# Kernel optimization log

Measured on AMD Instinct MI355X. Metric: run time of the kernel, lower is better.

Reference implementation:

```python
import jax, jax.numpy as jnp
import numpy as np

N_DELAYS = 512
N_SAMPLES = 2 ** 15  # 32768


def _interp_linear(x, out_size):
    # F.interpolate(mode='linear', align_corners=False) on [B, C, L]
    L = x.shape[-1]
    scale = L / out_size
    pos = (jnp.arange(out_size, dtype=jnp.float32) + 0.5) * scale - 0.5
    pos = jnp.clip(pos, 0.0, L - 1)
    i0 = jnp.floor(pos).astype(jnp.int32)
    i1 = jnp.minimum(i0 + 1, L - 1)
    w = (pos - i0).astype(x.dtype)
    return x[..., i0] * (1.0 - w) + x[..., i1] * w


def _interp_nearest(x, out_size):
    # F.interpolate(mode='nearest') on [B, C, L]: idx = floor(j * L/out)
    L = x.shape[-1]
    idx = jnp.clip(jnp.floor(jnp.arange(out_size) * (L / out_size)).astype(jnp.int32), 0, L - 1)
    return x[..., idx]


def setup_inputs() -> dict:
    key = jax.random.key(0)
    k1, k2, k3, k4, k5 = jax.random.split(key, 5)
    batch = 8
    impulse = jax.random.normal(k1, (batch, 128), dtype=jnp.float32)
    delay_selection = jax.random.normal(k2, (batch, N_DELAYS, 16), dtype=jnp.float32)
    damping = jax.random.normal(k3, (batch, 1), dtype=jnp.float32)
    filt = jax.random.normal(k4, (batch, 16), dtype=jnp.float32)
    # torch forward draws uniform(-1,1) noise; passed as input for determinism
    noise = jax.random.uniform(k5, (batch, 1, N_SAMPLES), dtype=jnp.float32, minval=-1.0, maxval=1.0)
    # comb-filter buffer: delays[i, ::i+1] = 1
    delays_np = np.zeros((N_DELAYS, N_SAMPLES), dtype=np.float32)
    for i in range(N_DELAYS):
        delays_np[i, ::i + 1] = 1.0
    delays = jnp.asarray(delays_np)
    return {"impulse": impulse, "delay_selection": delay_selection, "damping": damping,
            "filt": filt, "noise": noise, "delays": delays}


def reference(impulse, delay_selection, damping, filt, noise, delays):
    batch = delay_selection.shape[0]
    n_delays, n_samples = delays.shape
    n_frames = filt.shape[-1]

    # filter spectrum envelope: sigmoid -> linear upsample to n_samples//2 -> pad 1
    f = jax.nn.sigmoid(filt).reshape(-1, 1, n_frames)
    f = _interp_linear(f, n_samples // 2)
    filt_spec = jnp.pad(f, ((0, 0), (0, 0), (0, 1)))  # [B,1,n_samples//2+1]

    # impulse: squared envelope upsampled, modulating uniform noise
    imp = impulse.reshape(batch, 1, -1) ** 2
    imp = _interp_linear(imp, n_samples) * noise  # [B,1,n_samples]

    # damping: powers = linspace(1, 1, n_frames) == ones (faithful to source)
    damp = jax.nn.sigmoid(damping.reshape(batch, 1)) * 0.9999
    powers = jnp.linspace(1.0, float(damp.shape[-1]), n_frames)
    damp = damp[:, :, None] ** powers[None, None, :]  # [B,1,n_frames]
    damp = _interp_nearest(damp, n_samples)  # [B,1,n_samples]

    # sparse comb selection: softmax over delays, nearest upsample, weighted sum
    ds = jax.nn.softmax(delay_selection.reshape(batch, n_delays, -1), axis=1)
    ds = _interp_nearest(ds, n_samples)  # [B,n_delays,n_samples]
    d = jnp.einsum('bdn,dn->bn', ds, delays)[:, None, :] * damp  # [B,1,n_samples]

    # FFT convolution
    delay_spec = jnp.fft.rfft(d, axis=-1, norm='ortho')
    impulse_spec = jnp.fft.rfft(imp, axis=-1, norm='ortho')
    spec = delay_spec * impulse_spec * filt_spec
    final = jnp.fft.irfft(spec, n=n_samples, axis=-1, norm='ortho')
    return final
```

## Files before the change

kernel.cpp:

```cpp
#include <hip/hip_runtime.h>
#include <math.h>

#define NSAMP 32768
#define NDEL  512
#define NFR   16
#define BATCH 8
#define TWO_PI 6.283185307179586f

__device__ __forceinline__ float2 cmul(float2 a, float2 b) {
    return make_float2(a.x*b.x - a.y*b.y, a.x*b.y + a.y*b.x);
}
__device__ __forceinline__ float2 cadd(float2 a, float2 b){ return make_float2(a.x+b.x, a.y+b.y); }
__device__ __forceinline__ float2 csub(float2 a, float2 b){ return make_float2(a.x-b.x, a.y-b.y); }
__device__ __forceinline__ float2 crot(float2 z, float sign){ return make_float2(-sign*z.y, sign*z.x); }

__device__ __forceinline__ int phi(int i){ return i + (i >> 3); }

__device__ __forceinline__ void bfly8(const float2 v[8], float sign, float2 X[8]) {
    const float S2 = 0.70710678118654752f;
    float2 t0 = cadd(v[0], v[4]), t1 = csub(v[0], v[4]);
    float2 t2 = cadd(v[2], v[6]), t3 = crot(csub(v[2], v[6]), sign);
    float2 E0 = cadd(t0, t2), E1 = cadd(t1, t3), E2 = csub(t0, t2), E3 = csub(t1, t3);
    float2 u0 = cadd(v[1], v[5]), u1 = csub(v[1], v[5]);
    float2 u2 = cadd(v[3], v[7]), u3 = crot(csub(v[3], v[7]), sign);
    float2 O0 = cadd(u0, u2), O1 = cadd(u1, u3), O2 = csub(u0, u2), O3 = csub(u1, u3);
    float2 c1 = make_float2( S2, sign*S2);
    float2 c3 = make_float2(-S2, sign*S2);
    float2 w1o = cmul(c1, O1);
    float2 w2o = crot(O2, sign);
    float2 w3o = cmul(c3, O3);
    X[0]=cadd(E0,O0);  X[4]=csub(E0,O0);
    X[1]=cadd(E1,w1o); X[5]=csub(E1,w1o);
    X[2]=cadd(E2,w2o); X[6]=csub(E2,w2o);
    X[3]=cadd(E3,w3o); X[7]=csub(E3,w3o);
}

__device__ __forceinline__ void twiddle_q(float2 v[8], float ang1) {
    float sa, ca; __sincosf(ang1, &sa, &ca);
    float2 w1 = make_float2(ca, sa), wq = w1;
#pragma unroll
    for (int q = 1; q < 8; ++q) { v[q] = cmul(v[q], wq); wq = cmul(wq, w1); }
}

__global__ void build_kernel(const float* __restrict__ impulse,
                             const float* __restrict__ dsel,
                             const float* __restrict__ damping,
                             const float* __restrict__ noise,
                             float2* __restrict__ At) {
    const int b   = blockIdx.x >> 6;
    const int f   = (blockIdx.x >> 2) & 15;
    const int sub = blockIdx.x & 3;
    const int tid = threadIdx.x;
    __shared__ float Wrow[NDEL];
    __shared__ float dl[512];
    __shared__ float red[64];

    float v[8], m = -1e30f;
#pragma unroll
    for (int k = 0; k < 8; ++k) {
        v[k] = dsel[(b*NDEL + tid + 64*k)*NFR + f];
        m = fmaxf(m, v[k]);
    }
    red[tid] = m;
    __syncthreads();
    for (int off = 32; off > 0; off >>= 1) {
        if (tid < off) red[tid] = fmaxf(red[tid], red[tid+off]);
        __syncthreads();
    }
    float M = red[0];
    __syncthreads();
    float e[8], s = 0.0f;
#pragma unroll
    for (int k = 0; k < 8; ++k) { e[k] = expf(v[k] - M); s += e[k]; }
    red[tid] = s;
    __syncthreads();
    for (int off = 32; off > 0; off >>= 1) {
        if (tid < off) red[tid] += red[tid+off];
        __syncthreads();
    }
    float S = red[0];
    float damp = 1.0f/(1.0f + expf(-damping[b])) * 0.9999f;
    float scale = damp / S;
#pragma unroll
    for (int k = 0; k < 8; ++k) Wrow[tid + 64*k] = e[k] * scale;
    for (int k = tid; k < 512; k += 64) dl[k] = 0.0f;
    __syncthreads();

    const unsigned start = ((unsigned)f << 11) + ((unsigned)sub << 9);
    const float fstart = (float)start;

    for (unsigned t = 1; t < 64; ++t) {
        float wt = Wrow[t-1];
        unsigned q0 = (unsigned)(__fdividef(fstart, (float)t));
        unsigned n0 = q0 * t;
        while (n0 < start) n0 += t;
        while (n0 >= start + t) n0 -= t;
        for (unsigned i = (n0 - start) + (unsigned)tid * t; i < 512u; i += 64u * t)
            atomicAdd(&dl[i], wt);
    }
    for (unsigned t = 64u + (unsigned)tid; t <= 512u; t += 64u) {
        float wt = Wrow[t-1];
        unsigned q0 = (unsigned)(__fdividef(fstart, (float)t));
        unsigned n0 = q0 * t;
        while (n0 < start) n0 += t;
        while (n0 >= start + t) n0 -= t;
        for (unsigned i = n0 - start; i < 512u; i += t)
            atomicAdd(&dl[i], wt);
    }
    __syncthreads();

    const int n1base = (int)(start >> 6);
    float2* op = At + b*NSAMP + tid*512 + n1base;
#pragma unroll
    for (int q = 0; q < 8; ++q) {
        int n = (int)start + tid + 64*q;
        float pos = (n + 0.5f) * (1.0f/256.0f) - 0.5f;
        pos = fminf(fmaxf(pos, 0.0f), 127.0f);
        int i0 = (int)pos;
        float w = pos - (float)i0;
        int i1 = (i0 + 1 > 127) ? 127 : i0 + 1;
        float x0 = impulse[b*128 + i0]; x0 *= x0;
        float x1 = impulse[b*128 + i1]; x1 *= x1;
        float iv = (x0*(1.0f - w) + x1*w) * noise[b*NSAMP + n];
        op[q] = make_float2(dl[tid + 64*q], iv);
    }
}

__global__ void fft512_kernel(const float2* __restrict__ src,
                              float2* __restrict__ dst,
                              const float* __restrict__ filt,
                              float sign) {
    const int j  = threadIdx.x;
    const int s  = blockIdx.x >> 6;
    const int n2 = blockIdx.x & 63;
    __shared__ float2 buf[2][576];
    __shared__ float fs[NFR];
    if (filt && j < NFR)
        fs[j] = 1.0f/(1.0f + expf(-filt[s*NFR + j]));
    __syncthreads();

    const float2* sp = src + s * NSAMP;
    float2 v[8], X[8];
    if (!filt) {
#pragma unroll
        for (int q = 0; q < 8; ++q) v[q] = sp[n2*512 + j + 64*q];
    } else {
        const float SCALE = 1.0f / (32768.0f * 181.01933598375618f);
        const int prow = (64 - n2) & 63;
#pragma unroll
        for (int q = 0; q < 8; ++q) {
            int n1 = j + 64*q;
            int m  = 64*n1 + n2;
            float2 Zk = sp[n2*512 + n1];
            int pcol = n2 ? (511 - n1) : ((512 - n1) & 511);
            float2 Zr = sp[prow*512 + pcol];
            float2 Zrc = make_float2(Zr.x, -Zr.y);
            float2 D = make_float2(0.5f*(Zk.x + Zrc.x), 0.5f*(Zk.y + Zrc.y));
            float2 df = make_float2(Zk.x - Zrc.x, Zk.y - Zrc.y);
            float2 I = make_float2(0.5f*df.y, -0.5f*df.x);
            int jjb = (m <= NSAMP - m) ? m : NSAMP - m;
            float fv = 0.0f;
            if (jjb < NSAMP/2) {
                float pos = (jjb + 0.5f) * (1.0f/1024.0f) - 0.5f;
                pos = fminf(fmaxf(pos, 0.0f), 15.0f);
                int i0 = (int)pos;
                float w = pos - (float)i0;
                int i1 = (i0 + 1 > 15) ? 15 : i0 + 1;
                fv = fs[i0]*(1.0f - w) + fs[i1]*w;
            }
            float2 spc = cmul(D, I);
            float g = fv * SCALE;
            v[q] = make_float2(spc.x * g, spc.y * g);
        }
    }

    bfly8(v, sign, X);
#pragma unroll
    for (int r = 0; r < 8; ++r) buf[0][phi(8*j + r)] = X[r];
    __syncthreads();
#pragma unroll
    for (int q = 0; q < 8; ++q) v[q] = buf[0][phi(j + 64*q)];
    int jm = j & 7;
    twiddle_q(v, sign * TWO_PI * (float)jm * (1.0f/64.0f));
    bfly8(v, sign, X);
#pragma unroll
    for (int r = 0; r < 8; ++r) buf[1][phi(((j>>3)<<6) + jm + (r<<3))] = X[r];
    __syncthreads();
#pragma unroll
    for (int q = 0; q < 8; ++q) v[q] = buf[1][phi(j + 64*q)];
    twiddle_q(v, sign * TWO_PI * (float)j * (1.0f/512.0f));
    bfly8(v, sign, X);

    float2* dp = dst + s * NSAMP + n2 * 512;
#pragma unroll
    for (int r = 0; r < 8; ++r) {
        int k1 = j + 64*r;
        int pr = (n2 * k1) & (NSAMP - 1);
        float sa, ca; __sincosf(sign * TWO_PI * (float)pr * (1.0f/32768.0f), &sa, &ca);
        dp[k1] = cmul(X[r], make_float2(ca, sa));
    }
}

__global__ void fft64_kernel(const float2* __restrict__ src,
                             float2* __restrict__ dstT,
                             float* __restrict__ out_real,
                             float sign) {
    const int l = threadIdx.x;
    const int c = l & 7, jj = l >> 3;
    const int s = blockIdx.x >> 6;
    const int k1base = (blockIdx.x & 63) << 3;
    __shared__ float2 buf[576];

    const float2* sp = src + s * NSAMP;
    float2 v[8], X[8];
#pragma unroll
    for (int q = 0; q < 8; ++q) v[q] = sp[(jj + 8*q)*512 + k1base + c];

    bfly8(v, sign, X);
#pragma unroll
    for (int r = 0; r < 8; ++r) buf[phi(c*64 + jj*8 + r)] = X[r];
    __syncthreads();
#pragma unroll
    for (int q = 0; q < 8; ++q) v[q] = buf[phi(c*64 + jj + 8*q)];
    twiddle_q(v, sign * TWO_PI * (float)jj * (1.0f/64.0f));
    bfly8(v, sign, X);

    const int k1 = k1base + c;
    if (out_real) {
        float* op = out_real + s * NSAMP + k1;
#pragma unroll
        for (int r = 0; r < 8; ++r) op[512*(jj + 8*r)] = X[r].x;
    } else {
        float2* dp = dstT + s * NSAMP + (k1 & 63)*512 + (k1 >> 6) + 8*jj;
#pragma unroll
        for (int r = 0; r < 8; ++r) dp[64*r] = X[r];
    }
}

extern "C" void kernel_launch(void* const* d_in, const int* in_sizes, int n_in,
                              void* d_out, int out_size, void* d_ws, size_t ws_size,
                              hipStream_t stream) {
    const float* impulse = (const float*)d_in[0];
    const float* dsel    = (const float*)d_in[1];
    const float* damping = (const float*)d_in[2];
    const float* filt    = (const float*)d_in[3];
    const float* noise   = (const float*)d_in[4];
    float* out = (float*)d_out;

    float2* A = (float2*)d_ws;
    float2* B = A + BATCH * NSAMP;

    build_kernel<<<dim3(512), dim3(64), 0, stream>>>(impulse, dsel, damping, noise, A);
    fft512_kernel<<<dim3(512), dim3(64), 0, stream>>>(A, B, nullptr, -1.0f);
    fft64_kernel <<<dim3(512), dim3(64), 0, stream>>>(B, A, nullptr, -1.0f);
    fft512_kernel<<<dim3(512), dim3(64), 0, stream>>>(A, B, filt, 1.0f);
    fft64_kernel <<<dim3(512), dim3(64), 0, stream>>>(B, nullptr, out, 1.0f);
}
```

Before: 135.9 us.

## Fuse five FFT-pipeline kernels into one cooperative kernel with grid syncs

Replaces the five separate kernel launches (build, two forward FFT passes, two inverse FFT passes) with a single cooperative kernel that runs each phase as a device function and separates phases with grid-wide syncs. Shared memory is unified into one buffer reused across phases. This removes per-launch overhead and inter-kernel gaps, at the cost of grid barriers and the requirement that all 512 blocks be co-resident.

```diff
diff --git a/kernel.cpp b/kernel.cpp
--- a/kernel.cpp
+++ b/kernel.cpp
@@ -1,5 +1,8 @@
 #include <hip/hip_runtime.h>
+#include <hip/hip_cooperative_groups.h>
 #include <math.h>
+
+namespace cg = cooperative_groups;
 
 #define NSAMP 32768
 #define NDEL  512
@@ -42,18 +45,18 @@
     for (int q = 1; q < 8; ++q) { v[q] = cmul(v[q], wq); wq = cmul(wq, w1); }
 }
 
-__global__ void build_kernel(const float* __restrict__ impulse,
-                             const float* __restrict__ dsel,
-                             const float* __restrict__ damping,
-                             const float* __restrict__ noise,
-                             float2* __restrict__ At) {
-    const int b   = blockIdx.x >> 6;
-    const int f   = (blockIdx.x >> 2) & 15;
-    const int sub = blockIdx.x & 3;
+__device__ void phase_build(int task, const float* __restrict__ impulse,
+                            const float* __restrict__ dsel,
+                            const float* __restrict__ damping,
+                            const float* __restrict__ noise,
+                            float2* __restrict__ At, float2* sbuf) {
+    const int b   = task >> 6;
+    const int f   = (task >> 2) & 15;
+    const int sub = task & 3;
     const int tid = threadIdx.x;
-    __shared__ float Wrow[NDEL];
-    __shared__ float dl[512];
-    __shared__ float red[64];
+    float* Wrow = (float*)sbuf;
+    float* dl   = Wrow + 512;
+    float* red  = dl + 512;
 
     float v[8], m = -1e30f;
 #pragma unroll
@@ -126,15 +129,15 @@
     }
 }
 
-__global__ void fft512_kernel(const float2* __restrict__ src,
-                              float2* __restrict__ dst,
-                              const float* __restrict__ filt,
-                              float sign) {
+__device__ void phase_fft512(int task, const float2* __restrict__ src,
+                             float2* __restrict__ dst,
+                             const float* __restrict__ filt,
+                             float sign, float2* sbuf, float* fs) {
     const int j  = threadIdx.x;
-    const int s  = blockIdx.x >> 6;
-    const int n2 = blockIdx.x & 63;
-    __shared__ float2 buf[2][576];
-    __shared__ float fs[NFR];
+    const int s  = task >> 6;
+    const int n2 = task & 63;
+    float2* buf0 = sbuf;
+    float2* buf1 = sbuf + 576;
     if (filt && j < NFR)
         fs[j] = 1.0f/(1.0f + expf(-filt[s*NFR + j]));
     __syncthreads();
@@ -176,18 +179,18 @@
 
     bfly8(v, sign, X);
 #pragma unroll
-    for (int r = 0; r < 8; ++r) buf[0][phi(8*j + r)] = X[r];
-    __syncthreads();
-#pragma unroll
-    for (int q = 0; q < 8; ++q) v[q] = buf[0][phi(j + 64*q)];
+    for (int r = 0; r < 8; ++r) buf0[phi(8*j + r)] = X[r];
+    __syncthreads();
+#pragma unroll
+    for (int q = 0; q < 8; ++q) v[q] = buf0[phi(j + 64*q)];
     int jm = j & 7;
     twiddle_q(v, sign * TWO_PI * (float)jm * (1.0f/64.0f));
     bfly8(v, sign, X);
 #pragma unroll
-    for (int r = 0; r < 8; ++r) buf[1][phi(((j>>3)<<6) + jm + (r<<3))] = X[r];
-    __syncthreads();
-#pragma unroll
-    for (int q = 0; q < 8; ++q) v[q] = buf[1][phi(j + 64*q)];
+    for (int r = 0; r < 8; ++r) buf1[phi(((j>>3)<<6) + jm + (r<<3))] = X[r];
+    __syncthreads();
+#pragma unroll
+    for (int q = 0; q < 8; ++q) v[q] = buf1[phi(j + 64*q)];
     twiddle_q(v, sign * TWO_PI * (float)j * (1.0f/512.0f));
     bfly8(v, sign, X);
 
@@ -201,15 +204,15 @@
     }
 }
 
-__global__ void fft64_kernel(const float2* __restrict__ src,
-                             float2* __restrict__ dstT,
-                             float* __restrict__ out_real,
-                             float sign) {
+__device__ void phase_fft64(int task, const float2* __restrict__ src,
+                            float2* __restrict__ dstT,
+                            float* __restrict__ out_real,
+                            float sign, float2* sbuf) {
     const int l = threadIdx.x;
     const int c = l & 7, jj = l >> 3;
-    const int s = blockIdx.x >> 6;
-    const int k1base = (blockIdx.x & 63) << 3;
-    __shared__ float2 buf[576];
+    const int s = task >> 6;
+    const int k1base = (task & 63) << 3;
+    float2* buf = sbuf;
 
     const float2* sp = src + s * NSAMP;
     float2 v[8], X[8];
@@ -235,6 +238,27 @@
 #pragma unroll
         for (int r = 0; r < 8; ++r) dp[64*r] = X[r];
     }
+}
+
+__global__ void __launch_bounds__(64)
+fused_kernel(const float* __restrict__ impulse, const float* __restrict__ dsel,
+             const float* __restrict__ damping, const float* __restrict__ filt,
+             const float* __restrict__ noise, float2* __restrict__ A,
+             float2* __restrict__ B, float* __restrict__ out) {
+    cg::grid_group grid = cg::this_grid();
+    __shared__ float2 sbuf[1152];
+    __shared__ float  sfs[NFR];
+    const int task = blockIdx.x;
+
+    phase_build(task, impulse, dsel, damping, noise, A, sbuf);
+    __threadfence(); grid.sync();
+    phase_fft512(task, A, B, nullptr, -1.0f, sbuf, sfs);
+    __threadfence(); grid.sync();
+    phase_fft64(task, B, A, nullptr, -1.0f, sbuf);
+    __threadfence(); grid.sync();
+    phase_fft512(task, A, B, filt, 1.0f, sbuf, sfs);
+    __threadfence(); grid.sync();
+    phase_fft64(task, B, nullptr, out, 1.0f, sbuf);
 }
 
 extern "C" void kernel_launch(void* const* d_in, const int* in_sizes, int n_in,
@@ -250,9 +274,8 @@
     float2* A = (float2*)d_ws;
     float2* B = A + BATCH * NSAMP;
 
-    build_kernel<<<dim3(512), dim3(64), 0, stream>>>(impulse, dsel, damping, noise, A);
-    fft512_kernel<<<dim3(512), dim3(64), 0, stream>>>(A, B, nullptr, -1.0f);
-    fft64_kernel <<<dim3(512), dim3(64), 0, stream>>>(B, A, nullptr, -1.0f);
-    fft512_kernel<<<dim3(512), dim3(64), 0, stream>>>(A, B, filt, 1.0f);
-    fft64_kernel <<<dim3(512), dim3(64), 0, stream>>>(B, nullptr, out, 1.0f);
-}
+    void* args[] = {(void*)&impulse, (void*)&dsel, (void*)&damping, (void*)&filt,
+                    (void*)&noise,   (void*)&A,    (void*)&B,       (void*)&out};
+    hipLaunchCooperativeKernel((const void*)fused_kernel, dim3(512), dim3(64),
+                               args, 0, stream);
+}
```

New measurement: 440.1 us. 224% more time.

## Fuse forward fft64, spectral multiply and inverse fft64 into one kernel

Applied to the files above, without the earlier changes.

Combines the forward 64-point column FFT, the real-signal split and spectrum multiply with the filter envelope, and the inverse 64-point column FFT into a single kernel. Each block pairs columns k with their mirror columns so the conjugate-symmetric partner is available in shared memory. This removes one kernel launch and a full round-trip of the intermediate complex buffer through global memory. The final inverse 512-point FFT now writes the real output directly. The trade-off is more complex indexing and special-case handling for the DC and Nyquist columns, which carries some correctness risk.

```diff
diff --git a/kernel.cpp b/kernel.cpp
--- a/kernel.cpp
+++ b/kernel.cpp
@@ -126,39 +126,101 @@
     }
 }
 
-__global__ void fft512_kernel(const float2* __restrict__ src,
-                              float2* __restrict__ dst,
-                              const float* __restrict__ filt,
-                              float sign) {
+__global__ void fft512_fwd_kernel(const float2* __restrict__ src,
+                                  float2* __restrict__ dst) {
     const int j  = threadIdx.x;
     const int s  = blockIdx.x >> 6;
     const int n2 = blockIdx.x & 63;
     __shared__ float2 buf[2][576];
-    __shared__ float fs[NFR];
-    if (filt && j < NFR)
-        fs[j] = 1.0f/(1.0f + expf(-filt[s*NFR + j]));
-    __syncthreads();
+    const float sign = -1.0f;
 
     const float2* sp = src + s * NSAMP;
     float2 v[8], X[8];
-    if (!filt) {
-#pragma unroll
-        for (int q = 0; q < 8; ++q) v[q] = sp[n2*512 + j + 64*q];
-    } else {
-        const float SCALE = 1.0f / (32768.0f * 181.01933598375618f);
-        const int prow = (64 - n2) & 63;
-#pragma unroll
-        for (int q = 0; q < 8; ++q) {
-            int n1 = j + 64*q;
-            int m  = 64*n1 + n2;
-            float2 Zk = sp[n2*512 + n1];
-            int pcol = n2 ? (511 - n1) : ((512 - n1) & 511);
-            float2 Zr = sp[prow*512 + pcol];
+#pragma unroll
+    for (int q = 0; q < 8; ++q) v[q] = sp[n2*512 + j + 64*q];
+
+    bfly8(v, sign, X);
+#pragma unroll
+    for (int r = 0; r < 8; ++r) buf[0][phi(8*j + r)] = X[r];
+    __syncthreads();
+#pragma unroll
+    for (int q = 0; q < 8; ++q) v[q] = buf[0][phi(j + 64*q)];
+    int jm = j & 7;
+    twiddle_q(v, sign * TWO_PI * (float)jm * (1.0f/64.0f));
+    bfly8(v, sign, X);
+#pragma unroll
+    for (int r = 0; r < 8; ++r) buf[1][phi(((j>>3)<<6) + jm + (r<<3))] = X[r];
+    __syncthreads();
+#pragma unroll
+    for (int q = 0; q < 8; ++q) v[q] = buf[1][phi(j + 64*q)];
+    twiddle_q(v, sign * TWO_PI * (float)j * (1.0f/512.0f));
+    bfly8(v, sign, X);
+
+    float2* dp = dst + s * NSAMP + n2 * 512;
+#pragma unroll
+    for (int r = 0; r < 8; ++r) {
+        int k1 = j + 64*r;
+        int pr = (n2 * k1) & (NSAMP - 1);
+        float sa, ca; __sincosf(sign * TWO_PI * (float)pr * (1.0f/32768.0f), &sa, &ca);
+        dp[k1] = cmul(X[r], make_float2(ca, sa));
+    }
+}
+
+__global__ void mega_kernel(const float2* __restrict__ G,
+                            float2* __restrict__ H,
+                            const float* __restrict__ filt) {
+    const int l  = threadIdx.x;
+    const int cc = l & 7, jj = l >> 3;
+    const int s  = blockIdx.x >> 6;
+    const int g  = blockIdx.x & 63;
+    __shared__ float2 Z[8][65];
+    __shared__ float2 buf[576];
+    __shared__ float fs[NFR];
+    __shared__ int cols[8];
+
+    if (l < NFR) fs[l] = 1.0f/(1.0f + expf(-filt[s*NFR + l]));
+    if (l < 8) {
+        int col;
+        if (l < 4)        col = 4*g + l;
+        else if (g == 0)  col = (l == 4) ? 256 : 512 - (l - 4);
+        else              col = 512 - 4*g - (l - 4);
+        cols[l] = col;
+    }
+    __syncthreads();
+
+    const float2* sp = G + s * NSAMP;
+    const int mycol = cols[cc];
+    float2 v[8], X[8];
+
+#pragma unroll
+    for (int q = 0; q < 8; ++q) v[q] = sp[(jj + 8*q)*512 + mycol];
+    bfly8(v, -1.0f, X);
+#pragma unroll
+    for (int r = 0; r < 8; ++r) buf[phi(cc*64 + jj*8 + r)] = X[r];
+    __syncthreads();
+#pragma unroll
+    for (int q = 0; q < 8; ++q) v[q] = buf[phi(cc*64 + jj + 8*q)];
+    twiddle_q(v, -TWO_PI * (float)jj * (1.0f/64.0f));
+    bfly8(v, -1.0f, X);
+#pragma unroll
+    for (int r = 0; r < 8; ++r) Z[cc][jj + 8*r] = X[r];
+    __syncthreads();
+
+    const float SCALE = 1.0f / (32768.0f * 181.01933598375618f);
+#pragma unroll
+    for (int it = 0; it < 4; ++it) {
+        int c  = l & 3;
+        int k2 = (l >> 2) + 16*it;
+        if (!(g == 0 && c == 0)) {
+            int col = cols[c];
+            float2 Zk = Z[c][k2];
+            float2 Zr = Z[c+4][63 - k2];
             float2 Zrc = make_float2(Zr.x, -Zr.y);
             float2 D = make_float2(0.5f*(Zk.x + Zrc.x), 0.5f*(Zk.y + Zrc.y));
             float2 df = make_float2(Zk.x - Zrc.x, Zk.y - Zrc.y);
             float2 I = make_float2(0.5f*df.y, -0.5f*df.x);
-            int jjb = (m <= NSAMP - m) ? m : NSAMP - m;
+            int k = col + 512*k2;
+            int jjb = (k <= NSAMP - k) ? k : NSAMP - k;
             float fv = 0.0f;
             if (jjb < NSAMP/2) {
                 float pos = (jjb + 0.5f) * (1.0f/1024.0f) - 0.5f;
@@ -168,11 +230,97 @@
                 int i1 = (i0 + 1 > 15) ? 15 : i0 + 1;
                 fv = fs[i0]*(1.0f - w) + fs[i1]*w;
             }
-            float2 spc = cmul(D, I);
-            float g = fv * SCALE;
-            v[q] = make_float2(spc.x * g, spc.y * g);
+            float2 spec = cmul(D, I);
+            float gs = fv * SCALE;
+            Z[c][k2]        = make_float2( spec.x*gs,  spec.y*gs);
+            Z[c+4][63 - k2] = make_float2( spec.x*gs, -spec.y*gs);
         }
     }
+    if (g == 0) {
+        if (l <= 32) {
+            int k2 = l, k2p = (64 - k2) & 63;
+            float2 Zk = Z[0][k2];
+            float2 Zr = Z[0][k2p];
+            float2 Zrc = make_float2(Zr.x, -Zr.y);
+            float2 D = make_float2(0.5f*(Zk.x + Zrc.x), 0.5f*(Zk.y + Zrc.y));
+            float2 df = make_float2(Zk.x - Zrc.x, Zk.y - Zrc.y);
+            float2 I = make_float2(0.5f*df.y, -0.5f*df.x);
+            int k = 512*k2;
+            int jjb = (k <= NSAMP - k) ? k : NSAMP - k;
+            float fv = 0.0f;
+            if (jjb < NSAMP/2) {
+                float pos = (jjb + 0.5f) * (1.0f/1024.0f) - 0.5f;
+                pos = fminf(fmaxf(pos, 0.0f), 15.0f);
+                int i0 = (int)pos;
+                float w = pos - (float)i0;
+                int i1 = (i0 + 1 > 15) ? 15 : i0 + 1;
+                fv = fs[i0]*(1.0f - w) + fs[i1]*w;
+            }
+            float2 spec = cmul(D, I);
+            float gs = fv * SCALE;
+            Z[0][k2]  = make_float2( spec.x*gs,  spec.y*gs);
+            Z[0][k2p] = make_float2( spec.x*gs, -spec.y*gs);
+        }
+        if (l < 32) {
+            int k2 = l, k2p = 63 - k2;
+            float2 Zk = Z[4][k2];
+            float2 Zr = Z[4][k2p];
+            float2 Zrc = make_float2(Zr.x, -Zr.y);
+            float2 D = make_float2(0.5f*(Zk.x + Zrc.x), 0.5f*(Zk.y + Zrc.y));
+            float2 df = make_float2(Zk.x - Zrc.x, Zk.y - Zrc.y);
+            float2 I = make_float2(0.5f*df.y, -0.5f*df.x);
+            int k = 256 + 512*k2;
+            int jjb = (k <= NSAMP - k) ? k : NSAMP - k;
+            float fv = 0.0f;
+            {
+                float pos = (jjb + 0.5f) * (1.0f/1024.0f) - 0.5f;
+                pos = fminf(fmaxf(pos, 0.0f), 15.0f);
+                int i0 = (int)pos;
+                float w = pos - (float)i0;
+                int i1 = (i0 + 1 > 15) ? 15 : i0 + 1;
+                fv = fs[i0]*(1.0f - w) + fs[i1]*w;
+            }
+            float2 spec = cmul(D, I);
+            float gs = fv * SCALE;
+            Z[4][k2]  = make_float2( spec.x*gs,  spec.y*gs);
+            Z[4][k2p] = make_float2( spec.x*gs, -spec.y*gs);
+        }
+    }
+    __syncthreads();
+
+#pragma unroll
+    for (int q = 0; q < 8; ++q) v[q] = Z[cc][jj + 8*q];
+    bfly8(v, 1.0f, X);
+#pragma unroll
+    for (int r = 0; r < 8; ++r) buf[phi(cc*64 + jj*8 + r)] = X[r];
+    __syncthreads();
+#pragma unroll
+    for (int q = 0; q < 8; ++q) v[q] = buf[phi(cc*64 + jj + 8*q)];
+    twiddle_q(v, TWO_PI * (float)jj * (1.0f/64.0f));
+    bfly8(v, 1.0f, X);
+
+    float2* hp = H + s * NSAMP + mycol;
+#pragma unroll
+    for (int r = 0; r < 8; ++r) {
+        int n2 = jj + 8*r;
+        int pr = (n2 * mycol) & (NSAMP - 1);
+        float sa, ca; __sincosf(TWO_PI * (float)pr * (1.0f/32768.0f), &sa, &ca);
+        hp[n2*512] = cmul(X[r], make_float2(ca, sa));
+    }
+}
+
+__global__ void fft512_out_kernel(const float2* __restrict__ H,
+                                  float* __restrict__ out) {
+    const int j  = threadIdx.x;
+    const int s  = blockIdx.x >> 6;
+    const int n2 = blockIdx.x & 63;
+    __shared__ float2 buf[2][576];
+    const float sign = 1.0f;
+
+    const float2* sp = H + s * NSAMP;
+    float2 v[8], X[8];
+#pragma unroll
+    for (int q = 0; q < 8; ++q) v[q] = sp[n2*512 + j + 64*q];
 
     bfly8(v, sign, X);
 #pragma unroll
@@ -191,50 +339,9 @@
     twiddle_q(v, sign * TWO_PI * (float)j * (1.0f/512.0f));
     bfly8(v, sign, X);
 
-    float2* dp = dst + s * NSAMP + n2 * 512;
-#pragma unroll
-    for (int r = 0; r < 8; ++r) {
-        int k1 = j + 64*r;
-        int pr = (n2 * k1) & (NSAMP - 1);
-        float sa, ca; __sincosf(sign * TWO_PI * (float)pr * (1.0f/32768.0f), &sa, &ca);
-        dp[k1] = cmul(X[r], make_float2(ca, sa));
-    }
-}
-
-__global__ void fft64_kernel(const float2* __restrict__ src,
-                             float2* __restrict__ dstT,
-                             float* __restrict__ out_real,
-                             float sign) {
-    const int l = threadIdx.x;
-    const int c = l & 7, jj = l >> 3;
-    const int s = blockIdx.x >> 6;
-    const int k1base = (blockIdx.x & 63) << 3;
-    __shared__ float2 buf[576];
-
-    const float2* sp = src + s * NSAMP;
-    float2 v[8], X[8];
-#pragma unroll
-    for (int q = 0; q < 8; ++q) v[q] = sp[(jj + 8*q)*512 + k1base + c];
-
-    bfly8(v, sign, X);
-#pragma unroll
-    for (int r = 0; r < 8; ++r) buf[phi(c*64 + jj*8 + r)] = X[r];
-    __syncthreads();
-#pragma unroll
-    for (int q = 0; q < 8; ++q) v[q] = buf[phi(c*64 + jj + 8*q)];
-    twiddle_q(v, sign * TWO_PI * (float)jj * (1.0f/64.0f));
-    bfly8(v, sign, X);
-
-    const int k1 = k1base + c;
-    if (out_real) {
-        float* op = out_real + s * NSAMP + k1;
-#pragma unroll
-        for (int r = 0; r < 8; ++r) op[512*(jj + 8*r)] = X[r].x;
-    } else {
-        float2* dp = dstT + s * NSAMP + (k1 & 63)*512 + (k1 >> 6) + 8*jj;
-#pragma unroll
-        for (int r = 0; r < 8; ++r) dp[64*r] = X[r];
-    }
+    float* op = out + s * NSAMP + n2;
+#pragma unroll
+    for (int r = 0; r < 8; ++r) op[64*j + 4096*r] = X[r].x;
 }
 
 extern "C" void kernel_launch(void* const* d_in, const int* in_sizes, int n_in,
@@ -250,9 +357,8 @@
     float2* A = (float2*)d_ws;
     float2* B = A + BATCH * NSAMP;
 
-    build_kernel<<<dim3(512), dim3(64), 0, stream>>>(impulse, dsel, damping, noise, A);
-    fft512_kernel<<<dim3(512), dim3(64), 0, stream>>>(A, B, nullptr, -1.0f);
-    fft64_kernel <<<dim3(512), dim3(64), 0, stream>>>(B, A, nullptr, -1.0f);
-    fft512_kernel<<<dim3(512), dim3(64), 0, stream>>>(A, B, filt, 1.0f);
-    fft64_kernel <<<dim3(512), dim3(64), 0, stream>>>(B, nullptr, out, 1.0f);
-}
+    build_kernel    <<<dim3(512), dim3(64), 0, stream>>>(impulse, dsel, damping, noise, A);
+    fft512_fwd_kernel<<<dim3(512), dim3(64), 0, stream>>>(A, B);
+    mega_kernel     <<<dim3(512), dim3(64), 0, stream>>>(B, A, filt);
+    fft512_out_kernel<<<dim3(512), dim3(64), 0, stream>>>(A, out);
+}
```

After: 133.9 us. Within noise of the previous version (-1.5%).
